# Performance work log

Measured on AMD Instinct MI355X. Metric: run time of the kernel, lower is better.

The kernel has to match this reference:

```python
import jax, jax.numpy as jnp
import numpy as np
import math

D_K = 8  # = n_wires; one input value encoded per wire


def setup_inputs() -> dict:
    key = jax.random.key(0)
    k1, k2, k3, k4 = jax.random.split(key, 4)
    B, S, E = 4, 2048, 1024
    x = jax.random.normal(k1, (B, S, E), dtype=jnp.float32)
    theta = jax.random.normal(k2, (D_K,), dtype=jnp.float32)  # shared RX params (one ModuleList reused per head)
    W = jax.random.normal(k3, (E, E), dtype=jnp.float32) * (1.0 / math.sqrt(E))
    b = jax.random.normal(k4, (E,), dtype=jnp.float32) * 0.01
    return {"x": x, "theta": theta, "W": W, "b": b}


def reference(x, theta, W, b):
    B, S, E = x.shape
    dk = theta.shape[0]
    H = E // dk
    # Quantum circuit collapse: RX(x_i) then RX(theta_i) on |0>, measure PauliZ
    # on each wire of a product state -> <Z_i> = cos(x_i + theta_i).
    proj = x.reshape(B, S, H, dk)
    q_out = jnp.cos(proj + theta)  # theta broadcast over (B,S,H)
    # NOTE: faithful to original — attention is over the HEAD axis: (B,S,H,H)
    attn = jnp.einsum('bshd,bsgd->bshg', q_out, q_out) / math.sqrt(dk)
    attn = jax.nn.softmax(attn, axis=-1)  # dropout is identity at inference
    out = jnp.einsum('bshg,bsgd->bshd', attn, q_out)  # (B,S,H,dk)
    # faithful transpose(1,2).contiguous().view(B,S,E) reinterleave
    out = jnp.transpose(out, (0, 2, 1, 3)).reshape(B, S, E)
    return out @ W.T + b
```

## Files before the change

### kernel.cpp

```cpp
#include <hip/hip_runtime.h>
#include <hip/hip_bf16.h>
#include <stdint.h>

typedef __attribute__((ext_vector_type(8))) short bf16x8;
typedef __attribute__((ext_vector_type(4))) float f32x4;
typedef __attribute__((ext_vector_type(16))) float f32x16;
typedef __attribute__((ext_vector_type(2))) unsigned int uint32x2;
typedef __attribute__((address_space(3))) void lds_t;
typedef __attribute__((address_space(1))) void glb_t;

#define B_ 4
#define S_ 2048
#define E_ 1024
#define M_ (B_*S_)
#define QTS 152
#define PPB 2

static __device__ __forceinline__ ushort f2bf(float f) {
  uint32_t u = __float_as_uint(f);
  u += 0x7fffu + ((u >> 16) & 1u);
  return (ushort)(u >> 16);
}

static __device__ __forceinline__ uint32_t pk_bf16(float lo, float hi) {
  uint32_t r;
  asm("v_cvt_pk_bf16_f32 %0, %1, %2" : "=v"(r) : "v"(lo), "v"(hi));
  return r;
}
static __device__ __forceinline__ float fexp2(float x) {
  float r;
  asm("v_exp_f32 %0, %1" : "=v"(r) : "v"(x));
  return r;
}

static __device__ __forceinline__ void half_zip(uint32_t a, uint32_t b, bool convA,
                                                uint32_t& X, uint32_t& Y) {
  if (convA) {
    uint32x2 r = __builtin_amdgcn_permlane32_swap(b, a, false, false);
    Y = r[0]; X = r[1];
  } else {
    uint32x2 r = __builtin_amdgcn_permlane32_swap(a, b, false, false);
    X = r[0]; Y = r[1];
  }
}

__global__ __launch_bounds__(256) void qattn(const float* __restrict__ x,
                                             const float* __restrict__ theta,
                                             ushort* __restrict__ outr) {
  const int wave = threadIdx.x >> 6;
  const int lane = threadIdx.x & 63;
  const int l31 = lane & 31, hw = lane >> 5;

  const int bid = blockIdx.x;
  const int pair = (bid & 7) * 512 + (bid >> 3);

  __shared__ __align__(16) ushort qL[PPB][129 * 8];
  __shared__ __align__(16) ushort qT[PPB][16 * QTS];

  uint32x2 pr = __builtin_amdgcn_permlane32_swap((uint32_t)lane, (uint32_t)(lane + 1000),
                                                 false, false);
  const bool convA = (__builtin_amdgcn_readfirstlane((int)pr[0]) >= 1000);

  auto gen = [&](int bs_g, int sel) {
    ushort* qpg = qL[sel];
    ushort* qtg = qT[sel];
    const int h  = 32 * wave + (lane >> 1);
    const int dh = (lane & 1) * 4;
    const float4 xv = *(const float4*)(x + (size_t)bs_g * E_ + h * 8 + dh);
    float q[4];
    q[0] = __cosf(xv.x + theta[dh + 0]);
    q[1] = __cosf(xv.y + theta[dh + 1]);
    q[2] = __cosf(xv.z + theta[dh + 2]);
    q[3] = __cosf(xv.w + theta[dh + 3]);

    const float QS = 0.71419165f;
    uint2 pw;
    pw.x = pk_bf16(q[0] * QS, q[1] * QS);
    pw.y = pk_bf16(q[2] * QS, q[3] * QS);
    *(uint2*)(qpg + h * 8 + dh) = pw;

    #pragma unroll
    for (int j = 0; j < 4; ++j)
      qtg[(dh + j) * QTS + h] = f2bf(q[j]);
    qtg[(8 + dh) * QTS + h] = (ushort)0x3F80u;

    if (lane == 0) *(uint4*)(qpg + 128 * 8) = make_uint4(0, 0, 0, 0);
  };

  gen(pair * PPB + 0, 0);
  gen(pair * PPB + 1, 1);
  __syncthreads();
  __builtin_amdgcn_sched_barrier(0);

  const int hi = wave;

  #pragma unroll
  for (int pp = 0; pp < PPB; ++pp) {
    const ushort* qp = qL[pp];
    const ushort* qt = qT[pp];
    const int bs = pair * PPB + pp;
    const int b = bs >> 11, s = bs & 2047;

    bf16x8 aqv[4];
    #pragma unroll
    for (int gj = 0; gj < 4; ++gj) {
      const int arow = (lane < 32) ? (gj * 32 + l31) : 128;
      aqv[gj] = *(const bf16x8*)(qp + arow * 8);
    }
    const int brow = (lane < 32) ? (hi * 32 + l31) : 128;
    const bf16x8 bq = *(const bf16x8*)(qp + brow * 8);
    const ushort* qtb = qt + (l31 & 15) * QTS + hw * 8;

    f32x16 oaccA = {}, oaccB = {};

    #pragma unroll
    for (int gj = 0; gj < 4; ++gj) {
      f32x16 sc = {};
      sc = __builtin_amdgcn_mfma_f32_32x32x16_bf16(aqv[gj], bq, sc, 0, 0, 0);
      const bf16x8 fA = *(const bf16x8*)(qtb + (gj * 2 + 0) * 16);
      const bf16x8 fB = *(const bf16x8*)(qtb + (gj * 2 + 1) * 16);
      float pv[16];
      #pragma unroll
      for (int k = 0; k < 16; ++k) pv[k] = fexp2(sc[k]);
      #pragma unroll
      for (int sl = 0; sl < 2; ++sl) {
        const int pb = sl * 8;
        const uint32_t u = pk_bf16(pv[pb+0], pv[pb+1]);
        const uint32_t v = pk_bf16(pv[pb+2], pv[pb+3]);
        const uint32_t w = pk_bf16(pv[pb+4], pv[pb+5]);
        const uint32_t z = pk_bf16(pv[pb+6], pv[pb+7]);
        uint32_t f0, f1, f2, f3;
        half_zip(u, w, convA, f0, f2);
        half_zip(v, z, convA, f1, f3);
        uint32_t fr[4] = {f0, f1, f2, f3};
        if (gj < 2)
          oaccA = __builtin_amdgcn_mfma_f32_32x32x16_bf16((sl == 0) ? fA : fB,
                                                          *(const bf16x8*)fr, oaccA, 0, 0, 0);
        else
          oaccB = __builtin_amdgcn_mfma_f32_32x32x16_bf16((sl == 0) ? fA : fB,
                                                          *(const bf16x8*)fr, oaccB, 0, 0, 0);
      }
    }
    const f32x16 oacc = oaccA + oaccB;

    const int scol = s & 127, srow = s >> 7;
    const float inv = __builtin_amdgcn_rcpf(oacc[4]);
    const uint32_t o01 = pk_bf16(oacc[0] * inv, oacc[1] * inv);
    const uint32_t o23 = pk_bf16(oacc[2] * inv, oacc[3] * inv);
    const int h = hi * 32 + l31;
    const size_t row = (size_t)(b * 2048 + h * 16 + srow);
    *(uint2*)(outr + row * E_ + scol * 8 + hw * 4) = make_uint2(o01, o23);
  }
}

__global__ __launch_bounds__(256) void wconv(const float* __restrict__ W,
                                             ushort* __restrict__ Wb) {
  const int i = blockIdx.x * 256 + threadIdx.x;
  const float4 v = ((const float4*)W)[i];
  ushort4 o;
  o.x = f2bf(v.x); o.y = f2bf(v.y); o.z = f2bf(v.z); o.w = f2bf(v.w);
  ((ushort4*)Wb)[i] = o;
}

__global__ __launch_bounds__(256) void gemm_bt(const ushort* __restrict__ A,
                                               const ushort* __restrict__ Bw,
                                               const float* __restrict__ bias,
                                               float* __restrict__ C) {
  __shared__ __align__(16) ushort As[2][128 * 32];
  __shared__ __align__(16) ushort Bs[2][128 * 32];

  const int t = threadIdx.x;
  const int lane = t & 63;
  const int wavei = t >> 6;
  const int wr = wavei >> 1, wc = wavei & 1;
  const int lhi = lane >> 4, llo = lane & 15;
  const size_t ar0 = (size_t)blockIdx.x * 128;
  const size_t br0 = (size_t)blockIdx.y * 128;

  const int c0 = t, c1 = t + 256;
  const int r0 = c0 >> 2, kp0 = (c0 & 3) * 8;
  const int r1 = c1 >> 2, kp1 = (c1 & 3) * 8;

  auto stage = [&](int buf, int k0) {
    __builtin_amdgcn_global_load_lds((const glb_t*)(A  + (ar0 + r0) * E_ + k0 + kp0),
                                     (lds_t*)(As[buf] + c0 * 8), 16, 0, 0);
    __builtin_amdgcn_global_load_lds((const glb_t*)(A  + (ar0 + r1) * E_ + k0 + kp1),
                                     (lds_t*)(As[buf] + c1 * 8), 16, 0, 0);
    __builtin_amdgcn_global_load_lds((const glb_t*)(Bw + (br0 + r0) * E_ + k0 + kp0),
                                     (lds_t*)(Bs[buf] + c0 * 8), 16, 0, 0);
    __builtin_amdgcn_global_load_lds((const glb_t*)(Bw + (br0 + r1) * E_ + k0 + kp1),
                                     (lds_t*)(Bs[buf] + c1 * 8), 16, 0, 0);
  };

  f32x4 acc[4][4] = {};

  stage(0, 0);
  __syncthreads();

  for (int k0 = 0; k0 < E_; k0 += 32) {
    const int cur = (k0 >> 5) & 1;
    if (k0 + 32 < E_) stage(cur ^ 1, k0 + 32);

    bf16x8 af[4], bfr[4];
    #pragma unroll
    for (int i = 0; i < 4; ++i)
      af[i] = *(const bf16x8*)(As[cur] + (wr * 64 + i * 16 + llo) * 32 + lhi * 8);
    #pragma unroll
    for (int j = 0; j < 4; ++j)
      bfr[j] = *(const bf16x8*)(Bs[cur] + (wc * 64 + j * 16 + llo) * 32 + lhi * 8);

    #pragma unroll
    for (int i = 0; i < 4; ++i)
      #pragma unroll
      for (int j = 0; j < 4; ++j)
        acc[i][j] = __builtin_amdgcn_mfma_f32_16x16x32_bf16(af[i], bfr[j], acc[i][j], 0, 0, 0);

    __syncthreads();
  }

  #pragma unroll
  for (int j = 0; j < 4; ++j) {
    const int n = (int)br0 + wc * 64 + j * 16 + llo;
    const float bj = bias[n];
    #pragma unroll
    for (int i = 0; i < 4; ++i) {
      const int mb = (int)ar0 + wr * 64 + i * 16 + lhi * 4;
      #pragma unroll
      for (int r = 0; r < 4; ++r) {
        C[(size_t)(mb + r) * E_ + n] = acc[i][j][r] + bj;
      }
    }
  }
}

extern "C" void kernel_launch(void* const* d_in, const int* in_sizes, int n_in,
                              void* d_out, int out_size, void* d_ws, size_t ws_size,
                              hipStream_t stream) {
  const float* x     = (const float*)d_in[0];
  const float* theta = (const float*)d_in[1];
  const float* W     = (const float*)d_in[2];
  const float* bias  = (const float*)d_in[3];
  float* out = (float*)d_out;

  ushort* outr = (ushort*)d_ws;
  ushort* Wb   = (ushort*)((char*)d_ws + (size_t)M_ * E_ * 2);

  qattn<<<M_ / PPB, 256, 0, stream>>>(x, theta, outr);
  wconv<<<(E_ * E_) / (256 * 4), 256, 0, stream>>>(W, Wb);
  dim3 g(M_ / 128, E_ / 128);
  gemm_bt<<<g, 256, 0, stream>>>(outr, Wb, bias, out);
}
```

Measured before the change: 69.67 us.

## Process 8 positions per block and stage outputs in LDS for coalesced stores

Each block now handles 8 consecutive sequence positions instead of 2. All x loads are issued up front, and the per-position q tiles are packed into one shared buffer. Outputs are held in registers, transposed through LDS, and written as contiguous 128-byte chunks per head row instead of scattered 8-byte stores. This targets the poorly coalesced output write and amortises launch overhead, at the cost of more LDS per block, more registers and lower occupancy.

```diff
diff --git a/kernel.cpp b/kernel.cpp
--- a/kernel.cpp
+++ b/kernel.cpp
@@ -14,7 +14,9 @@
 #define E_ 1024
 #define M_ (B_*S_)
 #define QTS 152
-#define PPB 2
+#define PPB 8
+#define QSZ 3472
+#define WBS 140
 
 static __device__ __forceinline__ ushort f2bf(float f) {
   uint32_t u = __float_as_uint(f);
@@ -52,54 +54,55 @@
   const int l31 = lane & 31, hw = lane >> 5;
 
   const int bid = blockIdx.x;
-  const int pair = (bid & 7) * 512 + (bid >> 3);
-
-  __shared__ __align__(16) ushort qL[PPB][129 * 8];
-  __shared__ __align__(16) ushort qT[PPB][16 * QTS];
+  const int oct = (bid & 7) * 128 + (bid >> 3);
+  const int base = oct * PPB;
+  const int b = base >> 11;
+  const int s0 = base & 2047;
+  const int sr = s0 >> 7, scol0 = s0 & 127;
+
+  __shared__ __align__(16) ushort qALL[PPB * QSZ];
 
   uint32x2 pr = __builtin_amdgcn_permlane32_swap((uint32_t)lane, (uint32_t)(lane + 1000),
                                                  false, false);
   const bool convA = (__builtin_amdgcn_readfirstlane((int)pr[0]) >= 1000);
 
-  auto gen = [&](int bs_g, int sel) {
-    ushort* qpg = qL[sel];
-    ushort* qtg = qT[sel];
-    const int h  = 32 * wave + (lane >> 1);
-    const int dh = (lane & 1) * 4;
-    const float4 xv = *(const float4*)(x + (size_t)bs_g * E_ + h * 8 + dh);
+  const int gh  = 32 * wave + (lane >> 1);
+  const int gdh = (lane & 1) * 4;
+  float4 xv[PPB];
+  #pragma unroll
+  for (int pp = 0; pp < PPB; ++pp)
+    xv[pp] = *(const float4*)(x + (size_t)(base + pp) * E_ + gh * 8 + gdh);
+
+  const float QS = 0.71419165f;
+  #pragma unroll
+  for (int pp = 0; pp < PPB; ++pp) {
+    ushort* qpg = qALL + pp * QSZ;
+    ushort* qtg = qpg + 1040;
     float q[4];
-    q[0] = __cosf(xv.x + theta[dh + 0]);
-    q[1] = __cosf(xv.y + theta[dh + 1]);
-    q[2] = __cosf(xv.z + theta[dh + 2]);
-    q[3] = __cosf(xv.w + theta[dh + 3]);
-
-    const float QS = 0.71419165f;
+    q[0] = __cosf(xv[pp].x + theta[gdh + 0]);
+    q[1] = __cosf(xv[pp].y + theta[gdh + 1]);
+    q[2] = __cosf(xv[pp].z + theta[gdh + 2]);
+    q[3] = __cosf(xv[pp].w + theta[gdh + 3]);
     uint2 pw;
     pw.x = pk_bf16(q[0] * QS, q[1] * QS);
     pw.y = pk_bf16(q[2] * QS, q[3] * QS);
-    *(uint2*)(qpg + h * 8 + dh) = pw;
-
+    *(uint2*)(qpg + gh * 8 + gdh) = pw;
     #pragma unroll
     for (int j = 0; j < 4; ++j)
-      qtg[(dh + j) * QTS + h] = f2bf(q[j]);
-    qtg[(8 + dh) * QTS + h] = (ushort)0x3F80u;
-
+      qtg[(gdh + j) * QTS + gh] = f2bf(q[j]);
+    qtg[(8 + gdh) * QTS + gh] = (ushort)0x3F80u;
     if (lane == 0) *(uint4*)(qpg + 128 * 8) = make_uint4(0, 0, 0, 0);
-  };
-
-  gen(pair * PPB + 0, 0);
-  gen(pair * PPB + 1, 1);
+  }
   __syncthreads();
   __builtin_amdgcn_sched_barrier(0);
 
   const int hi = wave;
+  uint2 o_st[PPB];
 
   #pragma unroll
   for (int pp = 0; pp < PPB; ++pp) {
-    const ushort* qp = qL[pp];
-    const ushort* qt = qT[pp];
-    const int bs = pair * PPB + pp;
-    const int b = bs >> 11, s = bs & 2047;
+    const ushort* qp = qALL + pp * QSZ;
+    const ushort* qt = qp + 1040;
 
     bf16x8 aqv[4];
     #pragma unroll
@@ -143,13 +146,30 @@
     }
     const f32x16 oacc = oaccA + oaccB;
 
-    const int scol = s & 127, srow = s >> 7;
     const float inv = __builtin_amdgcn_rcpf(oacc[4]);
-    const uint32_t o01 = pk_bf16(oacc[0] * inv, oacc[1] * inv);
-    const uint32_t o23 = pk_bf16(oacc[2] * inv, oacc[3] * inv);
-    const int h = hi * 32 + l31;
-    const size_t row = (size_t)(b * 2048 + h * 16 + srow);
-    *(uint2*)(outr + row * E_ + scol * 8 + hw * 4) = make_uint2(o01, o23);
+    o_st[pp] = make_uint2(pk_bf16(oacc[0] * inv, oacc[1] * inv),
+                          pk_bf16(oacc[2] * inv, oacc[3] * inv));
+  }
+  __syncthreads();
+
+  char* wbuf = (char*)qALL;
+  {
+    const int h_loc = hi * 32 + l31;
+    #pragma unroll
+    for (int pp = 0; pp < PPB; ++pp)
+      *(uint2*)(wbuf + h_loc * WBS + pp * 16 + hw * 8) = o_st[pp];
+  }
+  __syncthreads();
+
+  {
+    const int t = (int)threadIdx.x;
+    const int h_loc = t >> 1, half = t & 1;
+    const size_t grow = (size_t)(b * 2048 + h_loc * 16 + sr);
+    ushort* gp = outr + grow * E_ + scol0 * 8 + half * 32;
+    const char* lp = wbuf + h_loc * WBS + half * 64;
+    #pragma unroll
+    for (int c = 0; c < 4; ++c)
+      *(uint4*)(gp + c * 8) = *(const uint4*)(lp + c * 16);
   }
 }
 
```

Measured after the change: 84.86 us. 1.22x slower.

## Process one (b,s) row per single-wave block, dropping block-wide syncs

Applied to the files above, without the earlier changes.

The qattn kernel now launches one 64-thread block per (b,s) row instead of 256-thread blocks covering two rows. A single wave builds both the scaled Q tile and the transposed V tile, each lane handling 16 inputs with packed stores, then loops over the four query-head groups itself. The V fragments are hoisted into registers once and reused across the loop. This removes __syncthreads and cross-wave LDS sharing, at the cost of more serial MFMA work per wave and more, smaller blocks.

```diff
diff --git a/kernel.cpp b/kernel.cpp
--- a/kernel.cpp
+++ b/kernel.cpp
@@ -14,7 +14,6 @@
 #define E_ 1024
 #define M_ (B_*S_)
 #define QTS 152
-#define PPB 2
 
 static __device__ __forceinline__ ushort f2bf(float f) {
   uint32_t u = __float_as_uint(f);
@@ -44,72 +43,78 @@
   }
 }
 
-__global__ __launch_bounds__(256) void qattn(const float* __restrict__ x,
-                                             const float* __restrict__ theta,
-                                             ushort* __restrict__ outr) {
-  const int wave = threadIdx.x >> 6;
+__global__ __launch_bounds__(64) void qattn(const float* __restrict__ x,
+                                            const float* __restrict__ theta,
+                                            ushort* __restrict__ outr) {
   const int lane = threadIdx.x & 63;
   const int l31 = lane & 31, hw = lane >> 5;
 
   const int bid = blockIdx.x;
-  const int pair = (bid & 7) * 512 + (bid >> 3);
-
-  __shared__ __align__(16) ushort qL[PPB][129 * 8];
-  __shared__ __align__(16) ushort qT[PPB][16 * QTS];
+  const int bs = (bid & 7) * 1024 + (bid >> 3);
+  const int b = bs >> 11, s = bs & 2047;
+
+  __shared__ __align__(16) ushort qp[129 * 8];
+  __shared__ __align__(16) ushort qt[16 * QTS];
 
   uint32x2 pr = __builtin_amdgcn_permlane32_swap((uint32_t)lane, (uint32_t)(lane + 1000),
                                                  false, false);
   const bool convA = (__builtin_amdgcn_readfirstlane((int)pr[0]) >= 1000);
 
-  auto gen = [&](int bs_g, int sel) {
-    ushort* qpg = qL[sel];
-    ushort* qtg = qT[sel];
-    const int h  = 32 * wave + (lane >> 1);
-    const int dh = (lane & 1) * 4;
-    const float4 xv = *(const float4*)(x + (size_t)bs_g * E_ + h * 8 + dh);
-    float q[4];
-    q[0] = __cosf(xv.x + theta[dh + 0]);
-    q[1] = __cosf(xv.y + theta[dh + 1]);
-    q[2] = __cosf(xv.z + theta[dh + 2]);
-    q[3] = __cosf(xv.w + theta[dh + 3]);
+  {
+    float th[8];
+    #pragma unroll
+    for (int d = 0; d < 8; ++d) th[d] = theta[d];
+
+    const float* xp = x + (size_t)bs * E_ + lane * 16;
+    float xr[16];
+    #pragma unroll
+    for (int i = 0; i < 4; ++i) {
+      const float4 v = ((const float4*)xp)[i];
+      xr[4*i+0] = v.x; xr[4*i+1] = v.y; xr[4*i+2] = v.z; xr[4*i+3] = v.w;
+    }
+    float q0[8], q1[8];
+    #pragma unroll
+    for (int d = 0; d < 8; ++d) {
+      q0[d] = __cosf(xr[d] + th[d]);
+      q1[d] = __cosf(xr[8 + d] + th[d]);
+    }
 
     const float QS = 0.71419165f;
-    uint2 pw;
-    pw.x = pk_bf16(q[0] * QS, q[1] * QS);
-    pw.y = pk_bf16(q[2] * QS, q[3] * QS);
-    *(uint2*)(qpg + h * 8 + dh) = pw;
-
-    #pragma unroll
-    for (int j = 0; j < 4; ++j)
-      qtg[(dh + j) * QTS + h] = f2bf(q[j]);
-    qtg[(8 + dh) * QTS + h] = (ushort)0x3F80u;
-
-    if (lane == 0) *(uint4*)(qpg + 128 * 8) = make_uint4(0, 0, 0, 0);
-  };
-
-  gen(pair * PPB + 0, 0);
-  gen(pair * PPB + 1, 1);
-  __syncthreads();
-  __builtin_amdgcn_sched_barrier(0);
-
-  const int hi = wave;
-
-  #pragma unroll
-  for (int pp = 0; pp < PPB; ++pp) {
-    const ushort* qp = qL[pp];
-    const ushort* qt = qT[pp];
-    const int bs = pair * PPB + pp;
-    const int b = bs >> 11, s = bs & 2047;
-
-    bf16x8 aqv[4];
-    #pragma unroll
-    for (int gj = 0; gj < 4; ++gj) {
-      const int arow = (lane < 32) ? (gj * 32 + l31) : 128;
-      aqv[gj] = *(const bf16x8*)(qp + arow * 8);
-    }
+    uint32_t qw[8];
+    #pragma unroll
+    for (int i = 0; i < 4; ++i) {
+      qw[i]     = pk_bf16(q0[2*i] * QS, q0[2*i+1] * QS);
+      qw[4 + i] = pk_bf16(q1[2*i] * QS, q1[2*i+1] * QS);
+    }
+    *(uint4*)(qp + (2*lane)     * 8) = *(uint4*)&qw[0];
+    *(uint4*)(qp + (2*lane + 1) * 8) = *(uint4*)&qw[4];
+    if (lane == 0) *(uint4*)(qp + 128 * 8) = make_uint4(0, 0, 0, 0);
+
+    #pragma unroll
+    for (int d = 0; d < 8; ++d)
+      *(uint32_t*)(qt + d * QTS + 2 * lane) = pk_bf16(q0[d], q1[d]);
+    *(uint32_t*)(qt + 8  * QTS + 2 * lane) = 0x3F803F80u;
+    *(uint32_t*)(qt + 12 * QTS + 2 * lane) = 0x3F803F80u;
+  }
+
+  bf16x8 aqv[4];
+  #pragma unroll
+  for (int gj = 0; gj < 4; ++gj) {
+    const int arow = (lane < 32) ? (gj * 32 + l31) : 128;
+    aqv[gj] = *(const bf16x8*)(qp + arow * 8);
+  }
+  const ushort* qtb = qt + (l31 & 15) * QTS + hw * 8;
+  bf16x8 pvf[8];
+  #pragma unroll
+  for (int ks = 0; ks < 8; ++ks)
+    pvf[ks] = *(const bf16x8*)(qtb + ks * 16);
+
+  const int scol = s & 127, srow = s >> 7;
+
+  #pragma unroll
+  for (int hi = 0; hi < 4; ++hi) {
     const int brow = (lane < 32) ? (hi * 32 + l31) : 128;
     const bf16x8 bq = *(const bf16x8*)(qp + brow * 8);
-    const ushort* qtb = qt + (l31 & 15) * QTS + hw * 8;
 
     f32x16 oaccA = {}, oaccB = {};
 
@@ -117,8 +122,6 @@
     for (int gj = 0; gj < 4; ++gj) {
       f32x16 sc = {};
       sc = __builtin_amdgcn_mfma_f32_32x32x16_bf16(aqv[gj], bq, sc, 0, 0, 0);
-      const bf16x8 fA = *(const bf16x8*)(qtb + (gj * 2 + 0) * 16);
-      const bf16x8 fB = *(const bf16x8*)(qtb + (gj * 2 + 1) * 16);
       float pv[16];
       #pragma unroll
       for (int k = 0; k < 16; ++k) pv[k] = fexp2(sc[k]);
@@ -134,16 +137,15 @@
         half_zip(v, z, convA, f1, f3);
         uint32_t fr[4] = {f0, f1, f2, f3};
         if (gj < 2)
-          oaccA = __builtin_amdgcn_mfma_f32_32x32x16_bf16((sl == 0) ? fA : fB,
+          oaccA = __builtin_amdgcn_mfma_f32_32x32x16_bf16(pvf[gj*2 + sl],
                                                           *(const bf16x8*)fr, oaccA, 0, 0, 0);
         else
-          oaccB = __builtin_amdgcn_mfma_f32_32x32x16_bf16((sl == 0) ? fA : fB,
+          oaccB = __builtin_amdgcn_mfma_f32_32x32x16_bf16(pvf[gj*2 + sl],
                                                           *(const bf16x8*)fr, oaccB, 0, 0, 0);
       }
     }
     const f32x16 oacc = oaccA + oaccB;
 
-    const int scol = s & 127, srow = s >> 7;
     const float inv = __builtin_amdgcn_rcpf(oacc[4]);
     const uint32_t o01 = pk_bf16(oacc[0] * inv, oacc[1] * inv);
     const uint32_t o23 = pk_bf16(oacc[2] * inv, oacc[3] * inv);
@@ -245,7 +247,7 @@
   ushort* outr = (ushort*)d_ws;
   ushort* Wb   = (ushort*)((char*)d_ws + (size_t)M_ * E_ * 2);
 
-  qattn<<<M_ / PPB, 256, 0, stream>>>(x, theta, outr);
+  qattn<<<M_, 64, 0, stream>>>(x, theta, outr);
   wconv<<<(E_ * E_) / (256 * 4), 256, 0, stream>>>(W, Wb);
   dim3 g(M_ / 128, E_ / 128);
   gemm_bt<<<g, 256, 0, stream>>>(outr, Wb, bias, out);
```

New measurement: 73.78 us. +5.9%, slower.
